# Optimization experiments

Measured on AMD Instinct MI355X. Metric: run time of the kernel, lower is better.

## Reference

```python
import jax, jax.numpy as jnp
import numpy as np

N_HEADS = 4
NEG_SLOPE = 0.2  # DGL GATConv default leaky_relu slope


def setup_inputs() -> dict:
    key = jax.random.key(0)
    ks = jax.random.split(key, 12)
    N, E = 50000, 800000
    in_dim, time_dim, out_dim = 128, 128, 128
    d_head = out_dim // N_HEADS
    in_total = in_dim + time_dim
    h = jax.random.normal(ks[0], (N, in_dim), jnp.float32)
    time_tensor = jax.random.uniform(ks[1], (E,), jnp.float32)
    src = jax.random.randint(ks[2], (E,), 0, N, jnp.int32)
    dst = jax.random.randint(ks[3], (E,), 0, N, jnp.int32)
    # TimeEncoding: Linear(1, time_dim) with xavier weight, zero bias
    w_t = jax.random.normal(ks[4], (time_dim, 1), jnp.float32) * (6.0 / (1 + time_dim)) ** 0.5
    b_t = jnp.zeros((time_dim,), jnp.float32)
    # GATConv params
    W_fc = jax.random.normal(ks[5], (N_HEADS * d_head, in_total), jnp.float32) * (2.0 / in_total) ** 0.5
    attn_l = jax.random.normal(ks[6], (N_HEADS, d_head), jnp.float32) * 0.1
    attn_r = jax.random.normal(ks[7], (N_HEADS, d_head), jnp.float32) * 0.1
    W_res = jax.random.normal(ks[8], (N_HEADS * d_head, in_total), jnp.float32) * (2.0 / in_total) ** 0.5
    bias = jnp.zeros((N_HEADS * d_head,), jnp.float32)
    return {"h": h, "time_tensor": time_tensor, "src": src, "dst": dst,
            "num_nodes": N, "w_t": w_t, "b_t": b_t, "W_fc": W_fc,
            "attn_l": attn_l, "attn_r": attn_r, "W_res": W_res, "bias": bias}


def reference(h, time_tensor, src, dst, num_nodes, w_t, b_t, W_fc, attn_l, attn_r, W_res, bias):
    N = num_nodes
    E = src.shape[0]
    # Time encoding: cos(W t + b), per edge -> [E, time_dim]
    time_emb = jnp.cos(time_tensor[:, None] * w_t[:, 0][None, :] + b_t[None, :])
    # Mailbox mean of concat([src h, time_emb]) per dst node.
    # mean(concat) == concat(mean, mean), so sum the two halves separately.
    ones = jnp.ones((E,), h.dtype)
    deg = jax.ops.segment_sum(ones, dst, num_segments=N)  # [N]
    sum_h = jax.ops.segment_sum(h[src], dst, num_segments=N)       # [N, in_dim]
    sum_t = jax.ops.segment_sum(time_emb, dst, num_segments=N)     # [N, time_dim]
    inv_deg = 1.0 / jnp.maximum(deg, 1.0)
    h_time = jnp.concatenate([sum_h, sum_t], axis=1) * inv_deg[:, None]  # [N, in+time]
    # GATConv (eval mode, no dropout)
    d_head = W_fc.shape[0] // N_HEADS
    feat = (h_time @ W_fc.T).reshape(N, N_HEADS, d_head)  # [N,H,D]
    el = jnp.sum(feat * attn_l[None], axis=-1)  # [N,H]
    er = jnp.sum(feat * attn_r[None], axis=-1)  # [N,H]
    e = el[src] + er[dst]                        # [E,H]
    e = jnp.where(e > 0, e, NEG_SLOPE * e)
    # edge softmax over incoming edges of each dst node
    m = jax.ops.segment_max(e, dst, num_segments=N)  # [N,H]
    m = jnp.where(jnp.isfinite(m), m, 0.0)
    ex = jnp.exp(e - m[dst])
    denom = jax.ops.segment_sum(ex, dst, num_segments=N)
    a = ex / jnp.maximum(denom[dst], 1e-9)           # [E,H]
    rst = jax.ops.segment_sum(a[:, :, None] * feat[src], dst, num_segments=N)  # [N,H,D]
    res = (h_time @ W_res.T).reshape(N, N_HEADS, d_head)
    out = rst + res + bias.reshape(1, N_HEADS, d_head)
    out = jax.nn.elu(out)
    return out.reshape(N, -1)  # [N, out_dim]
```

## Files before the change

kernel.cpp:

```cpp
#include <hip/hip_runtime.h>
#include <math.h>

#define NH 4
#define NEG_SLOPE 0.2f
#define BKT_SHIFT 8
#define EPB 4096
#define CBLK 8192
#define INV2PI 0.15915494309189535f
#define LOG2E  1.4426950408889634f

typedef __attribute__((ext_vector_type(8))) short bf16x8;
typedef __attribute__((ext_vector_type(4))) float f32x4;

__device__ __forceinline__ float blo(unsigned u) { return __uint_as_float(u << 16); }
__device__ __forceinline__ float bhi(unsigned u) { return __uint_as_float(u & 0xFFFF0000u); }
__device__ __forceinline__ unsigned short rne(float f) {
    unsigned u = __float_as_uint(f);
    u += 0x7FFFu + ((u >> 16) & 1u);
    return (unsigned short)(u >> 16);
}
__device__ __forceinline__ unsigned pack2(float a, float b) {
    return (unsigned)rne(a) | ((unsigned)rne(b) << 16);
}

__global__ __launch_bounds__(256) void k_prep(
    const float* __restrict__ h, unsigned* __restrict__ hbu, int n_pairs,
    const float* __restrict__ Wfc, const float* __restrict__ Wres,
    unsigned* __restrict__ wcat,
    const float* __restrict__ w_t, const float* __restrict__ b_t,
    float2* __restrict__ w_s, float2* __restrict__ b_s,
    const int* __restrict__ dst, int* __restrict__ bkt_cnt, int E, int NB, int EB) {
    __shared__ int cnt[256];
    int tid = threadIdx.x;
    int t = blockIdx.x * blockDim.x + tid;
    if (t < n_pairs) {
        float2 v = ((const float2*)h)[t];
        hbu[t] = pack2(v.x, v.y);
    }
    if (t < 32768) {
        int col = t >> 7, kk = t & 127;
        const float* srcp = (col < 128) ? (Wfc + (size_t)col * 256)
                                        : (Wres + (size_t)(col - 128) * 256);
        float2 v = ((const float2*)srcp)[kk];
        wcat[t] = pack2(v.x, v.y);
    }
    if (t < 64) {
        float2 wv = ((const float2*)w_t)[t];
        float2 bv = ((const float2*)b_t)[t];
        w_s[t] = make_float2(wv.x * INV2PI, wv.y * INV2PI);
        b_s[t] = make_float2(bv.x * INV2PI, bv.y * INV2PI);
    }
    if (blockIdx.x < (unsigned)EB) {
        cnt[tid] = 0;
        __syncthreads();
        int q0 = (blockIdx.x * CBLK) >> 2;
#pragma unroll
        for (int k = 0; k < CBLK / 1024; k++) {
            int qi = q0 + k * 256 + tid;
            int base = qi * 4;
            if (base + 3 < E) {
                int4 d = ((const int4*)dst)[qi];
                atomicAdd(&cnt[d.x >> BKT_SHIFT], 1);
                atomicAdd(&cnt[d.y >> BKT_SHIFT], 1);
                atomicAdd(&cnt[d.z >> BKT_SHIFT], 1);
                atomicAdd(&cnt[d.w >> BKT_SHIFT], 1);
            } else {
                for (int e = base; e < E; e++) atomicAdd(&cnt[dst[e] >> BKT_SHIFT], 1);
            }
        }
        __syncthreads();
        if (tid < NB) {
            int c = cnt[tid];
            if (c) atomicAdd(bkt_cnt + tid, c);
        }
    }
}

__global__ __launch_bounds__(256) void k_bktscan(
    const int* __restrict__ bkt_cnt, int* __restrict__ bkt_start,
    int* __restrict__ bkt_cursor, int* __restrict__ row_start,
    int NB, int E, int N) {
    __shared__ int wsum[4];
    int tid = threadIdx.x, lane = tid & 63, wid = tid >> 6;
    int v = (tid < NB) ? bkt_cnt[tid] : 0;
    int x = v;
#pragma unroll
    for (int off = 1; off < 64; off <<= 1) {
        int y = __shfl_up(x, off, 64);
        if (lane >= off) x += y;
    }
    if (lane == 63) wsum[wid] = x;
    __syncthreads();
    if (tid == 0) {
        int s = 0;
#pragma unroll
        for (int k = 0; k < 4; k++) { int tk = wsum[k]; wsum[k] = s; s += tk; }
    }
    __syncthreads();
    int excl = wsum[wid] + x - v;
    if (tid < NB) { bkt_start[tid] = excl; bkt_cursor[tid] = excl; }
    if (tid == 0) { bkt_start[NB] = E; row_start[N] = E; }
}

__global__ __launch_bounds__(256) void k_binscatter(
    const int* __restrict__ src, const int* __restrict__ dst,
    const float* __restrict__ tt, int* __restrict__ bkt_cursor,
    uint2* __restrict__ staged, int E, int NB) {
    __shared__ int cnt[1024];
    __shared__ int basep[1024];
    int e0 = blockIdx.x * EPB;
    int tid = threadIdx.x;
    for (int b = tid; b < NB; b += 256) cnt[b] = 0;
    __syncthreads();
#pragma unroll
    for (int k = 0; k < EPB / 256; k++) {
        int e = e0 + k * 256 + tid;
        if (e < E) atomicAdd(&cnt[dst[e] >> BKT_SHIFT], 1);
    }
    __syncthreads();
    for (int b = tid; b < NB; b += 256) {
        int c = cnt[b];
        basep[b] = (c > 0) ? atomicAdd(bkt_cursor + b, c) : 0;
        cnt[b] = 0;
    }
    __syncthreads();
#pragma unroll
    for (int k = 0; k < EPB / 256; k++) {
        int e = e0 + k * 256 + tid;
        if (e < E) {
            int d = dst[e];
            int b = d >> BKT_SHIFT;
            int r = atomicAdd(&cnt[b], 1);
            unsigned tq = min((unsigned)(tt[e] * 32768.0f), 32767u);
            staged[basep[b] + r] =
                make_uint2(((unsigned)src[e] << 15) | tq, (unsigned)(d & 255));
        }
    }
}

__global__ __launch_bounds__(256) void k_binsort(
    const uint2* __restrict__ staged, const int* __restrict__ bkt_start,
    int* __restrict__ row_start, unsigned* __restrict__ est, int N) {
    __shared__ int cnt[256];
    __shared__ int cur[256];
    __shared__ int wsum[4];
    int b = blockIdx.x;
    int n0 = b << BKT_SHIFT;
    int tid = threadIdx.x;
    cnt[tid] = 0;
    __syncthreads();
    int s0 = bkt_start[b], s1 = bkt_start[b + 1];
    for (int p = s0 + tid; p < s1; p += 256)
        atomicAdd(&cnt[staged[p].y], 1);
    __syncthreads();
    int lane = tid & 63, wid = tid >> 6;
    int v = cnt[tid];
    int x = v;
#pragma unroll
    for (int off = 1; off < 64; off <<= 1) {
        int y = __shfl_up(x, off, 64);
        if (lane >= off) x += y;
    }
    if (lane == 63) wsum[wid] = x;
    __syncthreads();
    if (tid == 0) {
        int s = 0;
#pragma unroll
        for (int k = 0; k < 4; k++) { int tk = wsum[k]; wsum[k] = s; s += tk; }
    }
    __syncthreads();
    int excl = s0 + wsum[wid] + x - v;
    cur[tid] = excl;
    if (n0 + tid < N) row_start[n0 + tid] = excl;
    __syncthreads();
    for (int p = s0 + tid; p < s1; p += 256) {
        uint2 vv = staged[p];
        int pos = atomicAdd(&cur[vv.y], 1);
        est[pos] = vv.x;
    }
}

__device__ __forceinline__ void agg_edge(unsigned u, const uint4* __restrict__ h4,
                                         int i, float4 wa, float4 wb, float4 ba, float4 bb,
                                         float* aH, float* aT) {
    int s = (int)(u >> 15);
    float t = (float)((u & 0x7FFFu)) * (1.0f / 32768.0f) + (0.5f / 32768.0f);
    uint4 hv = h4[(size_t)s * 16 + i];
    aH[0] += blo(hv.x); aH[1] += bhi(hv.x);
    aH[2] += blo(hv.y); aH[3] += bhi(hv.y);
    aH[4] += blo(hv.z); aH[5] += bhi(hv.z);
    aH[6] += blo(hv.w); aH[7] += bhi(hv.w);
    aT[0] += __builtin_amdgcn_cosf(fmaf(t, wa.x, ba.x));
    aT[1] += __builtin_amdgcn_cosf(fmaf(t, wa.y, ba.y));
    aT[2] += __builtin_amdgcn_cosf(fmaf(t, wa.z, ba.z));
    aT[3] += __builtin_amdgcn_cosf(fmaf(t, wa.w, ba.w));
    aT[4] += __builtin_amdgcn_cosf(fmaf(t, wb.x, bb.x));
    aT[5] += __builtin_amdgcn_cosf(fmaf(t, wb.y, bb.y));
    aT[6] += __builtin_amdgcn_cosf(fmaf(t, wb.z, bb.z));
    aT[7] += __builtin_amdgcn_cosf(fmaf(t, wb.w, bb.w));
}

__device__ __forceinline__ void attn_edge(unsigned u, const uint4* __restrict__ f4,
                                          int i, int hd, const float* __restrict__ el,
                                          float erh, float* acc, float& den) {
    int s = (int)(u >> 15);
    float elh = el[(size_t)s * 4 + hd];
    uint4 fv = f4[(size_t)s * 16 + i];
    float w = elh + erh; w = w > 0.f ? w : NEG_SLOPE * w;
    float ex = __builtin_amdgcn_exp2f(w);
    acc[0] = fmaf(ex, blo(fv.x), acc[0]); acc[1] = fmaf(ex, bhi(fv.x), acc[1]);
    acc[2] = fmaf(ex, blo(fv.y), acc[2]); acc[3] = fmaf(ex, bhi(fv.y), acc[3]);
    acc[4] = fmaf(ex, blo(fv.z), acc[4]); acc[5] = fmaf(ex, bhi(fv.z), acc[5]);
    acc[6] = fmaf(ex, blo(fv.w), acc[6]); acc[7] = fmaf(ex, bhi(fv.w), acc[7]);
    den += ex;
}

__global__ __launch_bounds__(256) void k_agg(
    const unsigned* __restrict__ hbu, const unsigned* __restrict__ est,
    const int* __restrict__ row_start,
    const float2* __restrict__ w_s, const float2* __restrict__ b_s,
    unsigned* __restrict__ htu, int N) {
    int n = blockIdx.x * 4 + (threadIdx.x >> 6);
    if (n >= N) return;
    int lane = threadIdx.x & 63;
    int g = lane >> 4, i = lane & 15;
    int rs = row_start[n], re = row_start[n + 1];
    const uint4* h4 = (const uint4*)hbu;
    float4 wa = ((const float4*)w_s)[2 * i], wb = ((const float4*)w_s)[2 * i + 1];
    float4 ba = ((const float4*)b_s)[2 * i], bb = ((const float4*)b_s)[2 * i + 1];
    float aH[8] = {}, aT[8] = {};
    int nb = (re - rs) >> 4;
    int e = rs + g;
    for (int j = 0; j < nb; j++, e += 16) {
        unsigned u0 = est[e];
        unsigned u1 = est[e + 4];
        unsigned u2 = est[e + 8];
        unsigned u3 = est[e + 12];
        agg_edge(u0, h4, i, wa, wb, ba, bb, aH, aT);
        agg_edge(u1, h4, i, wa, wb, ba, bb, aH, aT);
        agg_edge(u2, h4, i, wa, wb, ba, bb, aH, aT);
        agg_edge(u3, h4, i, wa, wb, ba, bb, aH, aT);
    }
    for (; e < re; e += 4)
        agg_edge(est[e], h4, i, wa, wb, ba, bb, aH, aT);
#pragma unroll
    for (int off = 16; off <= 32; off <<= 1) {
#pragma unroll
        for (int k = 0; k < 8; k++) {
            aH[k] += __shfl_xor(aH[k], off, 64);
            aT[k] += __shfl_xor(aT[k], off, 64);
        }
    }
    if (g == 0) {
        int deg = re - rs;
        float idg = (deg > 0) ? 1.0f / (float)deg : 1.0f;
        uint4* ht4 = (uint4*)htu;
        uint4 oh, ot;
        oh.x = pack2(aH[0] * idg, aH[1] * idg);
        oh.y = pack2(aH[2] * idg, aH[3] * idg);
        oh.z = pack2(aH[4] * idg, aH[5] * idg);
        oh.w = pack2(aH[6] * idg, aH[7] * idg);
        ot.x = pack2(aT[0] * idg, aT[1] * idg);
        ot.y = pack2(aT[2] * idg, aT[3] * idg);
        ot.z = pack2(aT[4] * idg, aT[5] * idg);
        ot.w = pack2(aT[6] * idg, aT[7] * idg);
        ht4[(size_t)n * 32 + i]      = oh;
        ht4[(size_t)n * 32 + 16 + i] = ot;
    }
}

__global__ __launch_bounds__(256) void k_gemm(
    const unsigned short* __restrict__ ht, const unsigned short* __restrict__ wcat,
    unsigned short* __restrict__ feat, float* __restrict__ res_out, int N) {
    int tid = threadIdx.x;
    int wave = tid >> 6, lane = tid & 63;
    int r = lane & 15, q = lane >> 4;
    int row0 = blockIdx.x * 16;
    int colbase = wave * 64;
    int gr = row0 + r; if (gr >= N) gr = N - 1;
    const bf16x8* a_base = (const bf16x8*)ht + (size_t)gr * 32;
    const bf16x8* bbase = (const bf16x8*)wcat + (size_t)(colbase + r) * 32;
    f32x4 acc[4] = {};
#pragma unroll
    for (int ks = 0; ks < 8; ks++) {
        bf16x8 a = a_base[ks * 4 + q];
        bf16x8 b[4];
#pragma unroll
        for (int ct = 0; ct < 4; ct++)
            b[ct] = bbase[(size_t)ct * (16 * 32) + ks * 4 + q];
#pragma unroll
        for (int ct = 0; ct < 4; ct++)
            acc[ct] = __builtin_amdgcn_mfma_f32_16x16x32_bf16(a, b[ct], acc[ct], 0, 0, 0);
    }
    bool featw = (colbase < 128);
#pragma unroll
    for (int ct = 0; ct < 4; ct++) {
        int col = colbase + ct * 16 + r;
#pragma unroll
        for (int reg = 0; reg < 4; reg++) {
            int row = row0 + q * 4 + reg;
            if (row >= N) continue;
            float v = acc[ct][reg];
            if (featw) feat[(size_t)row * 128 + col] = rne(v);
            else       res_out[(size_t)row * 128 + (col - 128)] = v;
        }
    }
}

__global__ void k_el_er(const unsigned* __restrict__ featu,
                        const float* __restrict__ attn_l, const float* __restrict__ attn_r,
                        float* __restrict__ el, float* __restrict__ er, int NH4) {
    int t = blockIdx.x * blockDim.x + threadIdx.x;
    if (t >= NH4) return;
    int n = t >> 2, hd = t & 3;
    const unsigned* f = featu + (size_t)n * 64 + hd * 16;
    const float2* al = (const float2*)(attn_l + hd * 32);
    const float2* ar = (const float2*)(attn_r + hd * 32);
    float sl = 0.f, sr = 0.f;
#pragma unroll
    for (int i = 0; i < 16; i++) {
        unsigned u = f[i];
        float f0 = blo(u), f1 = bhi(u);
        float2 a = al[i], b = ar[i];
        sl = fmaf(f0, a.x, fmaf(f1, a.y, sl));
        sr = fmaf(f0, b.x, fmaf(f1, b.y, sr));
    }
    el[t] = sl * LOG2E;
    er[t] = sr * LOG2E;
}

__global__ __launch_bounds__(256) void k_attn(
    const unsigned* __restrict__ est, const int* __restrict__ row_start,
    const float* __restrict__ el, const float* __restrict__ er,
    const unsigned* __restrict__ featu, const float* __restrict__ bias,
    float* __restrict__ out, int N) {
    int n = blockIdx.x * 4 + (threadIdx.x >> 6);
    if (n >= N) return;
    int lane = threadIdx.x & 63;
    int g = lane >> 4, i = lane & 15;
    int hd = i >> 2;
    int rs = row_start[n], re = row_start[n + 1];
    float erh = er[(size_t)n * 4 + hd];
    const uint4* f4 = (const uint4*)featu;
    float acc[8] = {};
    float den = 0.f;
    int nb = (re - rs) >> 4;
    int e = rs + g;
    for (int j = 0; j < nb; j++, e += 16) {
        unsigned u0 = est[e];
        unsigned u1 = est[e + 4];
        unsigned u2 = est[e + 8];
        unsigned u3 = est[e + 12];
        attn_edge(u0, f4, i, hd, el, erh, acc, den);
        attn_edge(u1, f4, i, hd, el, erh, acc, den);
        attn_edge(u2, f4, i, hd, el, erh, acc, den);
        attn_edge(u3, f4, i, hd, el, erh, acc, den);
    }
    for (; e < re; e += 4)
        attn_edge(est[e], f4, i, hd, el, erh, acc, den);
#pragma unroll
    for (int off = 16; off <= 32; off <<= 1) {
#pragma unroll
        for (int k = 0; k < 8; k++) acc[k] += __shfl_xor(acc[k], off, 64);
        den += __shfl_xor(den, off, 64);
    }
    if (g == 0) {
        float id = 1.0f / fmaxf(den, 1e-9f);
        float* op = out + (size_t)n * 128 + i * 8;
        const float* bp = bias + i * 8;
        float4 o0 = ((const float4*)op)[0], o1 = ((const float4*)op)[1];
        float4 b0 = ((const float4*)bp)[0], b1 = ((const float4*)bp)[1];
        float4 r0, r1;
        r0.x = fmaf(acc[0], id, o0.x + b0.x);
        r0.y = fmaf(acc[1], id, o0.y + b0.y);
        r0.z = fmaf(acc[2], id, o0.z + b0.z);
        r0.w = fmaf(acc[3], id, o0.w + b0.w);
        r1.x = fmaf(acc[4], id, o1.x + b1.x);
        r1.y = fmaf(acc[5], id, o1.y + b1.y);
        r1.z = fmaf(acc[6], id, o1.z + b1.z);
        r1.w = fmaf(acc[7], id, o1.w + b1.w);
        r0.x = r0.x > 0.f ? r0.x : (__expf(r0.x) - 1.0f);
        r0.y = r0.y > 0.f ? r0.y : (__expf(r0.y) - 1.0f);
        r0.z = r0.z > 0.f ? r0.z : (__expf(r0.z) - 1.0f);
        r0.w = r0.w > 0.f ? r0.w : (__expf(r0.w) - 1.0f);
        r1.x = r1.x > 0.f ? r1.x : (__expf(r1.x) - 1.0f);
        r1.y = r1.y > 0.f ? r1.y : (__expf(r1.y) - 1.0f);
        r1.z = r1.z > 0.f ? r1.z : (__expf(r1.z) - 1.0f);
        r1.w = r1.w > 0.f ? r1.w : (__expf(r1.w) - 1.0f);
        ((float4*)op)[0] = r0;
        ((float4*)op)[1] = r1;
    }
}

extern "C" void kernel_launch(void* const* d_in, const int* in_sizes, int n_in,
                              void* d_out, int out_size, void* d_ws, size_t ws_size,
                              hipStream_t stream) {
    const float* h     = (const float*)d_in[0];
    const float* tt    = (const float*)d_in[1];
    const int*   src   = (const int*)d_in[2];
    const int*   dst   = (const int*)d_in[3];
    const float* w_t   = (const float*)d_in[5];
    const float* b_t   = (const float*)d_in[6];
    const float* W_fc  = (const float*)d_in[7];
    const float* al    = (const float*)d_in[8];
    const float* ar    = (const float*)d_in[9];
    const float* W_res = (const float*)d_in[10];
    const float* bias  = (const float*)d_in[11];

    int N = in_sizes[0] / 128;
    int E = in_sizes[1];
    int NB = (N + 255) >> BKT_SHIFT;
    int EB = (E + CBLK - 1) / CBLK;

    char* ws = (char*)d_ws;
    size_t off = 0;
    auto alloc = [&](size_t bytes) { void* p = ws + off; off = (off + bytes + 15) & ~(size_t)15; return p; };
    unsigned* htu     = (unsigned*)alloc((size_t)N * 128 * 4);
    unsigned* hbu     = (unsigned*)alloc((size_t)N * 64 * 4);
    unsigned* featu   = (unsigned*)alloc((size_t)N * 64 * 4);
    unsigned* wcat    = (unsigned*)alloc(32768 * 4);
    float2*   w_s     = (float2*)alloc(64 * 8);
    float2*   b_s     = (float2*)alloc(64 * 8);
    float*    el      = (float*)alloc((size_t)N * NH * 4);
    float*    er      = (float*)alloc((size_t)N * NH * 4);
    int*      row_st  = (int*)alloc((size_t)(N + 1) * 4);
    int*      bkt_cur = (int*)alloc((size_t)NB * 4);
    int*      bkt_cnt = (int*)alloc((size_t)NB * 4);
    int*      bkt_sta = (int*)alloc((size_t)(NB + 1) * 4);
    unsigned* est     = (unsigned*)alloc((size_t)E * 4);
    uint2*    staged  = (uint2*)featu;

    hipMemsetAsync(bkt_cnt, 0, (size_t)NB * 4, stream);

    int prep_n = N * 64;
    hipLaunchKernelGGL(k_prep, dim3((prep_n + 255) / 256), dim3(256), 0, stream,
                       h, hbu, prep_n, W_fc, W_res, wcat, w_t, b_t, w_s, b_s,
                       dst, bkt_cnt, E, NB, EB);
    hipLaunchKernelGGL(k_bktscan, dim3(1), dim3(256), 0, stream,
                       bkt_cnt, bkt_sta, bkt_cur, row_st, NB, E, N);
    hipLaunchKernelGGL(k_binscatter, dim3((E + EPB - 1) / EPB), dim3(256), 0, stream,
                       src, dst, tt, bkt_cur, staged, E, NB);
    hipLaunchKernelGGL(k_binsort, dim3(NB), dim3(256), 0, stream,
                       staged, bkt_sta, row_st, est, N);
    hipLaunchKernelGGL(k_agg, dim3((N + 3) / 4), dim3(256), 0, stream,
                       hbu, est, row_st, w_s, b_s, htu, N);
    hipLaunchKernelGGL(k_gemm, dim3((N + 15) / 16), dim3(256), 0, stream,
                       (const unsigned short*)htu, (const unsigned short*)wcat,
                       (unsigned short*)featu, (float*)d_out, N);
    hipLaunchKernelGGL(k_el_er, dim3((N * NH + 255) / 256), dim3(256), 0, stream,
                       featu, al, ar, el, er, N * NH);
    hipLaunchKernelGGL(k_attn, dim3((N + 3) / 4), dim3(256), 0, stream,
                       est, row_st, el, er, featu, bias, (float*)d_out, N);
}
```

Before: 281.3 us.

## Tile GEMM over 64 rows with LDS-staged A and MFMA-ordered weight layout

The GEMM kernel now processes 64 rows per block instead of 16, staging the bf16 input rows in padded shared memory and computing a 4x4 grid of MFMA tiles per wave, so each weight fragment is reused four times. The weight packing in the prep kernel writes wcat in a fragment-contiguous order so each lane reads its B operand with a coalesced, lane-indexed load. The trade-offs are more accumulator registers per thread, about 33KB of LDS per block, and a quarter as many blocks. A local variable in the bucket-count loop is also renamed to avoid shadowing.

```diff
diff --git a/kernel.cpp b/kernel.cpp
--- a/kernel.cpp
+++ b/kernel.cpp
@@ -42,7 +42,10 @@
         const float* srcp = (col < 128) ? (Wfc + (size_t)col * 256)
                                         : (Wres + (size_t)(col - 128) * 256);
         float2 v = ((const float2*)srcp)[kk];
-        wcat[t] = pack2(v.x, v.y);
+        int s  = col >> 6, ct = (col >> 4) & 3, r = col & 15;
+        int ks = kk >> 4,  q  = (kk >> 2) & 3,  d = kk & 3;
+        int w2i = ((s * 32 + ks * 4 + ct) << 8) + ((q * 16 + r) << 2) + d;
+        wcat[w2i] = pack2(v.x, v.y);
     }
     if (t < 64) {
         float2 wv = ((const float2*)w_t)[t];
@@ -59,11 +62,11 @@
             int qi = q0 + k * 256 + tid;
             int base = qi * 4;
             if (base + 3 < E) {
-                int4 d = ((const int4*)dst)[qi];
-                atomicAdd(&cnt[d.x >> BKT_SHIFT], 1);
-                atomicAdd(&cnt[d.y >> BKT_SHIFT], 1);
-                atomicAdd(&cnt[d.z >> BKT_SHIFT], 1);
-                atomicAdd(&cnt[d.w >> BKT_SHIFT], 1);
+                int4 dd = ((const int4*)dst)[qi];
+                atomicAdd(&cnt[dd.x >> BKT_SHIFT], 1);
+                atomicAdd(&cnt[dd.y >> BKT_SHIFT], 1);
+                atomicAdd(&cnt[dd.z >> BKT_SHIFT], 1);
+                atomicAdd(&cnt[dd.w >> BKT_SHIFT], 1);
             } else {
                 for (int e = base; e < E; e++) atomicAdd(&cnt[dst[e] >> BKT_SHIFT], 1);
             }
@@ -270,39 +273,55 @@
 }
 
 __global__ __launch_bounds__(256) void k_gemm(
-    const unsigned short* __restrict__ ht, const unsigned short* __restrict__ wcat,
+    const unsigned short* __restrict__ ht, const unsigned* __restrict__ wcat,
     unsigned short* __restrict__ feat, float* __restrict__ res_out, int N) {
+    __shared__ __align__(16) unsigned short As[64 * 264];
     int tid = threadIdx.x;
+    int row0 = blockIdx.x * 64;
+    const uint4* src4 = (const uint4*)ht;
+    for (int idx = tid; idx < 64 * 32; idx += 256) {
+        int rl = idx >> 5, c16 = idx & 31;
+        int gr = row0 + rl; if (gr >= N) gr = N - 1;
+        uint4 v = src4[(size_t)gr * 32 + c16];
+        *(uint4*)(As + rl * 264 + c16 * 8) = v;
+    }
+    __syncthreads();
     int wave = tid >> 6, lane = tid & 63;
     int r = lane & 15, q = lane >> 4;
-    int row0 = blockIdx.x * 16;
     int colbase = wave * 64;
-    int gr = row0 + r; if (gr >= N) gr = N - 1;
-    const bf16x8* a_base = (const bf16x8*)ht + (size_t)gr * 32;
-    const bf16x8* bbase = (const bf16x8*)wcat + (size_t)(colbase + r) * 32;
-    f32x4 acc[4] = {};
+    const bf16x8* bbase = (const bf16x8*)wcat + (size_t)wave * 2048 + lane;
+    const unsigned short* abase = As + r * 264 + q * 8;
+    f32x4 acc[4][4] = {};
 #pragma unroll
     for (int ks = 0; ks < 8; ks++) {
-        bf16x8 a = a_base[ks * 4 + q];
-        bf16x8 b[4];
+        bf16x8 a[4], b[4];
+#pragma unroll
+        for (int rt = 0; rt < 4; rt++)
+            a[rt] = *(const bf16x8*)(abase + rt * (16 * 264) + ks * 32);
 #pragma unroll
         for (int ct = 0; ct < 4; ct++)
-            b[ct] = bbase[(size_t)ct * (16 * 32) + ks * 4 + q];
-#pragma unroll
-        for (int ct = 0; ct < 4; ct++)
-            acc[ct] = __builtin_amdgcn_mfma_f32_16x16x32_bf16(a, b[ct], acc[ct], 0, 0, 0);
+            b[ct] = bbase[(ks * 4 + ct) * 64];
+#pragma unroll
+        for (int rt = 0; rt < 4; rt++)
+#pragma unroll
+            for (int ct = 0; ct < 4; ct++)
+                acc[rt][ct] = __builtin_amdgcn_mfma_f32_16x16x32_bf16(a[rt], b[ct], acc[rt][ct], 0, 0, 0);
     }
     bool featw = (colbase < 128);
 #pragma unroll
-    for (int ct = 0; ct < 4; ct++) {
-        int col = colbase + ct * 16 + r;
-#pragma unroll
-        for (int reg = 0; reg < 4; reg++) {
-            int row = row0 + q * 4 + reg;
-            if (row >= N) continue;
-            float v = acc[ct][reg];
-            if (featw) feat[(size_t)row * 128 + col] = rne(v);
-            else       res_out[(size_t)row * 128 + (col - 128)] = v;
+    for (int rt = 0; rt < 4; rt++) {
+        int rb = row0 + rt * 16 + q * 4;
+#pragma unroll
+        for (int ct = 0; ct < 4; ct++) {
+            int col = colbase + ct * 16 + r;
+#pragma unroll
+            for (int reg = 0; reg < 4; reg++) {
+                int row = rb + reg;
+                if (row >= N) continue;
+                float v = acc[rt][ct][reg];
+                if (featw) feat[(size_t)row * 128 + col] = rne(v);
+                else       res_out[(size_t)row * 128 + (col - 128)] = v;
+            }
         }
     }
 }
@@ -444,8 +463,8 @@
                        staged, bkt_sta, row_st, est, N);
     hipLaunchKernelGGL(k_agg, dim3((N + 3) / 4), dim3(256), 0, stream,
                        hbu, est, row_st, w_s, b_s, htu, N);
-    hipLaunchKernelGGL(k_gemm, dim3((N + 15) / 16), dim3(256), 0, stream,
-                       (const unsigned short*)htu, (const unsigned short*)wcat,
+    hipLaunchKernelGGL(k_gemm, dim3((N + 63) / 64), dim3(256), 0, stream,
+                       (const unsigned short*)htu, wcat,
                        (unsigned short*)featu, (float*)d_out, N);
     hipLaunchKernelGGL(k_el_er, dim3((N * NH + 255) / 256), dim3(256), 0, stream,
                        featu, al, ar, el, er, N * NH);
```

Result: faster. 243.8 us (-13.3%).
